# Performance work log

Measured on AMD Instinct MI355X. Metric: run time of the kernel, lower is better.

The kernel has to match this reference:

```python
import jax, jax.numpy as jnp
import numpy as np

N_NODES = 100000
NEG_SLOPE = 0.2


def gat_conv(x, src, dst, W, a_src, a_dst, bias, concat):
    """PyG-style GATConv (eval mode, self-loops assumed already added).
    x: [N, F_in], src/dst: [E] (message flows src -> dst).
    W: [F_in, H*C], a_src/a_dst: [H, C], bias: [H*C] or [C].
    """
    H, C = a_src.shape
    N = x.shape[0]
    h = (x @ W).reshape(N, H, C)                      # [N, H, C]
    alpha_src = jnp.einsum('nhc,hc->nh', h, a_src)    # [N, H]
    alpha_dst = jnp.einsum('nhc,hc->nh', h, a_dst)    # [N, H]
    e = jax.nn.leaky_relu(alpha_src[src] + alpha_dst[dst], NEG_SLOPE)  # [E, H]
    # segment softmax over incoming edges of each dst node
    e_max = jax.ops.segment_max(e, dst, num_segments=N)
    e_exp = jnp.exp(e - e_max[dst])
    denom = jax.ops.segment_sum(e_exp, dst, num_segments=N)
    alpha = e_exp / (denom[dst] + 1e-16)              # [E, H]
    msg = h[src] * alpha[:, :, None]                  # [E, H, C]
    out = jax.ops.segment_sum(msg, dst, num_segments=N)  # [N, H, C]
    out = out.reshape(N, H * C) if concat else out.mean(axis=1)
    return out + bias


def add_self_loops(edge_index, n):
    loop = jnp.arange(n, dtype=edge_index.dtype)
    src = jnp.concatenate([edge_index[0], loop])
    dst = jnp.concatenate([edge_index[1], loop])
    return src, dst


def setup_inputs() -> dict:
    key = jax.random.key(0)
    ks = jax.random.split(key, 10)
    F_in, H1, C1, n_cls = 128, 8, 8, 40
    E = 1600000
    x = jax.random.normal(ks[0], (N_NODES, F_in), dtype=jnp.float32)
    edge_index = jax.random.randint(ks[1], (2, E), 0, N_NODES, dtype=jnp.int64)
    g = lambda k, shp, fan: jax.random.normal(k, shp, dtype=jnp.float32) * (1.0 / np.sqrt(fan))
    return {
        'x': x,
        'edge_index': edge_index,
        'W1': g(ks[2], (F_in, H1 * C1), F_in),
        'a_src1': g(ks[3], (H1, C1), C1),
        'a_dst1': g(ks[4], (H1, C1), C1),
        'b1': jnp.zeros((H1 * C1,), dtype=jnp.float32),
        'W2': g(ks[5], (H1 * C1, n_cls), H1 * C1),
        'a_src2': g(ks[6], (1, n_cls), n_cls),
        'a_dst2': g(ks[7], (1, n_cls), n_cls),
        'b2': jnp.zeros((n_cls,), dtype=jnp.float32),
    }


def reference(x, edge_index, W1, a_src1, a_dst1, b1, W2, a_src2, a_dst2, b2):
    src, dst = add_self_loops(edge_index, N_NODES)
    # dropout(p=0.6) layers are identity in eval mode
    h = gat_conv(x, src, dst, W1, a_src1, a_dst1, b1, concat=True)
    h = jax.nn.relu(h)
    out = gat_conv(h, src, dst, W2, a_src2, a_dst2, b2, concat=True)
    return out
```

## Files before the change

kernel.cpp:

```cpp
#include <hip/hip_runtime.h>
#include <math.h>

constexpr int NN     = 100000;
constexpr int E_BASE = 1600000;
constexpr int E_TOT  = E_BASE + NN;
constexpr int F_IN   = 128;
constexpr int F1     = 64;
constexpr int H1n    = 8;
constexpr int F2     = 40;

constexpr int BSHIFT    = 9;
constexpr int NB        = (NN + 511) >> BSHIFT;
constexpr int BCAP      = 12288;
constexpr int P1_BLOCKS = 256;
constexpr int EPB       = (E_TOT + P1_BLOCKS - 1) / P1_BLOCKS;
constexpr int L1_BLOCKS = (NN + 63) / 64;

__device__ __forceinline__ float lrelu(float v) { return fmaxf(v, 0.2f * v); }

__device__ __forceinline__ unsigned bpack(float a, float b) {
    unsigned ua = __float_as_uint(a) + 0x8000u;
    unsigned ub = __float_as_uint(b) + 0x8000u;
    return (ua >> 16) | (ub & 0xFFFF0000u);
}
__device__ __forceinline__ float blo(unsigned u) { return __uint_as_float(u << 16); }
__device__ __forceinline__ float bhi(unsigned u) { return __uint_as_float(u & 0xFFFF0000u); }

__global__ __launch_bounds__(256) void fused_l1p(const float* __restrict__ x,
                                                 const float* __restrict__ W1,
                                                 const float* __restrict__ a_src,
                                                 const float* __restrict__ a_dst,
                                                 unsigned* __restrict__ h1b,
                                                 float* __restrict__ as1,
                                                 float* __restrict__ ad1,
                                                 const int* __restrict__ src,
                                                 const int* __restrict__ dst,
                                                 int* __restrict__ bucket_cnt,
                                                 unsigned* __restrict__ store) {
    __shared__ __align__(16) unsigned char smraw[17408];
    int t = threadIdx.x;
    if (blockIdx.x < L1_BLOCKS) {
        float (*xs)[36] = (float(*)[36])smraw;
        float* wsld     = (float*)(smraw + 9216);
        int nb = blockIdx.x * 64;
        int ct = t & 15, nt = t >> 4;
        int rs = t >> 3, qs = t & 7;
        float acc[4][4] = {};
        for (int K0 = 0; K0 < F_IN; K0 += 32) {
            int r0 = min(nb + rs, NN - 1);
            int r1 = min(nb + rs + 32, NN - 1);
            float4 v0 = *(const float4*)&x[(size_t)r0 * F_IN + K0 + qs * 4];
            float4 v1 = *(const float4*)&x[(size_t)r1 * F_IN + K0 + qs * 4];
            *(float4*)&xs[rs][qs * 4] = v0;
            *(float4*)&xs[rs + 32][qs * 4] = v1;
            const float4* wsrc = (const float4*)&W1[(size_t)K0 * F1];
            *(float4*)&wsld[t * 4] = wsrc[t];
            *(float4*)&wsld[1024 + t * 4] = wsrc[256 + t];
            __syncthreads();
#pragma unroll 8
            for (int kk = 0; kk < 32; ++kk) {
                float4 w = *(const float4*)&wsld[kk * 64 + ct * 4];
                float x0 = xs[nt * 4 + 0][kk];
                float x1 = xs[nt * 4 + 1][kk];
                float x2 = xs[nt * 4 + 2][kk];
                float x3 = xs[nt * 4 + 3][kk];
                acc[0][0] = fmaf(x0, w.x, acc[0][0]); acc[0][1] = fmaf(x0, w.y, acc[0][1]);
                acc[0][2] = fmaf(x0, w.z, acc[0][2]); acc[0][3] = fmaf(x0, w.w, acc[0][3]);
                acc[1][0] = fmaf(x1, w.x, acc[1][0]); acc[1][1] = fmaf(x1, w.y, acc[1][1]);
                acc[1][2] = fmaf(x1, w.z, acc[1][2]); acc[1][3] = fmaf(x1, w.w, acc[1][3]);
                acc[2][0] = fmaf(x2, w.x, acc[2][0]); acc[2][1] = fmaf(x2, w.y, acc[2][1]);
                acc[2][2] = fmaf(x2, w.z, acc[2][2]); acc[2][3] = fmaf(x2, w.w, acc[2][3]);
                acc[3][0] = fmaf(x3, w.x, acc[3][0]); acc[3][1] = fmaf(x3, w.y, acc[3][1]);
                acc[3][2] = fmaf(x3, w.z, acc[3][2]); acc[3][3] = fmaf(x3, w.w, acc[3][3]);
            }
            __syncthreads();
        }
        float4 as4 = ((const float4*)a_src)[ct];
        float4 ds4 = ((const float4*)a_dst)[ct];
#pragma unroll
        for (int i = 0; i < 4; ++i) {
            int n = nb + nt * 4 + i;
            unsigned u0 = bpack(acc[i][0], acc[i][1]);
            unsigned u1 = bpack(acc[i][2], acc[i][3]);
            float ps = acc[i][0]*as4.x + acc[i][1]*as4.y + acc[i][2]*as4.z + acc[i][3]*as4.w;
            float pd = acc[i][0]*ds4.x + acc[i][1]*ds4.y + acc[i][2]*ds4.z + acc[i][3]*ds4.w;
            ps += __shfl_xor(ps, 1, 64);
            pd += __shfl_xor(pd, 1, 64);
            if (n < NN) {
                *(uint2*)&h1b[(size_t)n * 32 + ct * 2] = make_uint2(u0, u1);
                if (!(ct & 1)) {
                    as1[n * H1n + (ct >> 1)] = ps;
                    ad1[n * H1n + (ct >> 1)] = pd;
                }
            }
        }
    } else {
        int* bins  = (int*)smraw;
        int* basep = (int*)(smraw + NB * 4);
        for (int i = t; i < NB; i += 256) bins[i] = 0;
        __syncthreads();
        int pb = blockIdx.x - L1_BLOCKS;
        int e0 = pb * EPB;
        int e1 = min(e0 + EPB, E_TOT);
        for (int e = e0 + t; e < e1; e += 256) {
            int d = (e < E_BASE) ? dst[e] : (e - E_BASE);
            atomicAdd(&bins[d >> BSHIFT], 1);
        }
        __syncthreads();
        for (int i = t; i < NB; i += 256) {
            basep[i] = atomicAdd(&bucket_cnt[i], bins[i]);
            bins[i] = 0;
        }
        __syncthreads();
        for (int e = e0 + t; e < e1; e += 256) {
            int s, d;
            if (e < E_BASE) { s = src[e]; d = dst[e]; }
            else            { s = e - E_BASE; d = s; }
            int b = d >> BSHIFT;
            int p = atomicAdd(&bins[b], 1);
            store[(size_t)b * BCAP + basep[b] + p] = ((unsigned)s << 9) | (unsigned)(d & 511);
        }
    }
}

__global__ __launch_bounds__(256) void bucket_csr(const int* __restrict__ bucket_cnt,
                                                  const unsigned* __restrict__ store,
                                                  int* __restrict__ row_start,
                                                  int* __restrict__ csr_src) {
    __shared__ int cnt_l[512];
    __shared__ int incl[512];
    __shared__ int cur_l[512];
    __shared__ int sh_gbase;
    int b = blockIdx.x;
    int t = threadIdx.x;
    int cnt = bucket_cnt[b];
    int nlo = b << BSHIFT;
    int nodes = min(512, NN - nlo);
    cnt_l[t] = 0; cnt_l[t + 256] = 0;
    if (t < 64) {
        int partial = 0;
        for (int i = t; i < NB; i += 64)
            if (i < b) partial += bucket_cnt[i];
#pragma unroll
        for (int m = 1; m < 64; m <<= 1) partial += __shfl_xor(partial, m, 64);
        if (t == 0) {
            sh_gbase = partial;
            if (b == NB - 1) row_start[NN] = partial + cnt;
        }
    }
    __syncthreads();
    int gbase = sh_gbase;
    const unsigned* sp = store + (size_t)b * BCAP;
    for (int i = t; i < cnt; i += 256)
        atomicAdd(&cnt_l[sp[i] & 511], 1);
    __syncthreads();
    if (t < 64) {
        int run = 0;
        for (int c = 0; c < 512; c += 64) {
            int v = cnt_l[c + t];
#pragma unroll
            for (int off = 1; off < 64; off <<= 1) {
                int u = __shfl_up(v, off, 64);
                if (t >= off) v += u;
            }
            incl[c + t] = run + v;
            run = __shfl(run + v, 63, 64);
        }
    }
    __syncthreads();
    for (int j = t; j < 512; j += 256) {
        int start = gbase + incl[j] - cnt_l[j];
        cur_l[j] = start;
        if (j < nodes) row_start[nlo + j] = start;
    }
    __syncthreads();
    for (int i = t; i < cnt; i += 256) {
        unsigned ed = sp[i];
        int p = atomicAdd(&cur_l[ed & 511], 1);
        csr_src[p] = (int)(ed >> 9);
    }
}

__global__ void node_agg1(const int* __restrict__ row_start, const int* __restrict__ csr_src,
                          const float* __restrict__ as1, const float* __restrict__ ad1,
                          const unsigned* __restrict__ h1b, const float* __restrict__ b1,
                          float* __restrict__ out1r) {
    int n = blockIdx.x;
    int lane = threadIdx.x;
    int e8 = lane & 7, hp = lane >> 3;
    int il = lane & 31, q = lane >> 5;
    int hc = il >> 2;
    float adv = ad1[n * H1n + hp];
    int lo = row_start[n], hi = row_start[n + 1];
    float ssum = 0.f, acc0 = 0.f, acc1 = 0.f;
    for (int base = lo; base < hi; base += 8) {
        int idx = base + e8;
        bool valid = idx < hi;
        int s = csr_src[valid ? idx : (hi - 1)];
        float v = lrelu(as1[s * H1n + hp] + adv);
        float p = valid ? __expf(v) : 0.f;
        ssum += p;
#pragma unroll
        for (int j = 0; j < 4; ++j) {
            int e = 2 * j + q;
            int   sb = __shfl(s, e, 64);
            float pb = __shfl(p, (hc << 3) | e, 64);
            unsigned u = h1b[(size_t)sb * 32 + il];
            acc0 = fmaf(pb, blo(u), acc0);
            acc1 = fmaf(pb, bhi(u), acc1);
        }
    }
    ssum += __shfl_xor(ssum, 1, 64);
    ssum += __shfl_xor(ssum, 2, 64);
    ssum += __shfl_xor(ssum, 4, 64);
    float sh = __shfl(ssum, hc << 3, 64);
    float p0 = acc0 + __shfl(acc0, il | 32, 64);
    float p1 = acc1 + __shfl(acc1, il | 32, 64);
    if (lane < 32) {
        float r = 1.f / (sh + 1e-16f);
        float2 bv = ((const float2*)b1)[il];
        float2 o;
        o.x = fmaxf(fmaf(p0, r, bv.x), 0.f);
        o.y = fmaxf(fmaf(p1, r, bv.y), 0.f);
        ((float2*)(out1r + (size_t)n * F1))[il] = o;
    }
}

__global__ __launch_bounds__(256) void linear2(const float* __restrict__ out1r,
                                               const float* __restrict__ W2,
                                               const float* __restrict__ a_src2,
                                               const float* __restrict__ a_dst2,
                                               unsigned* __restrict__ h2a,
                                               unsigned* __restrict__ h2c,
                                               float* __restrict__ as2,
                                               float* __restrict__ ad2) {
    __shared__ float xs[128][65];
    __shared__ float ws[64 * 40];
    int t = threadIdx.x;
    int nb = blockIdx.x * 128;
    int colq = t & 15, rr = t >> 4;
#pragma unroll
    for (int i = 0; i < 8; ++i) {
        int r = rr + 16 * i;
        int g = min(nb + r, NN - 1);
        float4 v = *(const float4*)&out1r[(size_t)g * F1 + colq * 4];
        xs[r][colq * 4 + 0] = v.x; xs[r][colq * 4 + 1] = v.y;
        xs[r][colq * 4 + 2] = v.z; xs[r][colq * 4 + 3] = v.w;
    }
#pragma unroll
    for (int i = 0; i < 10; ++i) ws[t + 256 * i] = W2[t + 256 * i];
    __syncthreads();
    int ct = t & 7, nt = t >> 3;
    float acc[4][5] = {};
#pragma unroll 4
    for (int k = 0; k < F1; ++k) {
        float w0 = ws[k * 40 + ct * 5 + 0];
        float w1 = ws[k * 40 + ct * 5 + 1];
        float w2 = ws[k * 40 + ct * 5 + 2];
        float w3 = ws[k * 40 + ct * 5 + 3];
        float w4 = ws[k * 40 + ct * 5 + 4];
#pragma unroll
        for (int i = 0; i < 4; ++i) {
            float xv = xs[nt * 4 + i][k];
            acc[i][0] = fmaf(xv, w0, acc[i][0]);
            acc[i][1] = fmaf(xv, w1, acc[i][1]);
            acc[i][2] = fmaf(xv, w2, acc[i][2]);
            acc[i][3] = fmaf(xv, w3, acc[i][3]);
            acc[i][4] = fmaf(xv, w4, acc[i][4]);
        }
    }
    float aw[5], dw[5];
#pragma unroll
    for (int j = 0; j < 5; ++j) { aw[j] = a_src2[ct * 5 + j]; dw[j] = a_dst2[ct * 5 + j]; }
#pragma unroll
    for (int i = 0; i < 4; ++i) {
        int n = nb + nt * 4 + i;
        float vs = acc[i][0]*aw[0] + acc[i][1]*aw[1] + acc[i][2]*aw[2]
                 + acc[i][3]*aw[3] + acc[i][4]*aw[4];
        float vd = acc[i][0]*dw[0] + acc[i][1]*dw[1] + acc[i][2]*dw[2]
                 + acc[i][3]*dw[3] + acc[i][4]*dw[4];
        vs += __shfl_xor(vs, 1, 64); vs += __shfl_xor(vs, 2, 64); vs += __shfl_xor(vs, 4, 64);
        vd += __shfl_xor(vd, 1, 64); vd += __shfl_xor(vd, 2, 64); vd += __shfl_xor(vd, 4, 64);
        if (n < NN && ct == 0) { as2[n] = vs; ad2[n] = vd; }
    }
    __syncthreads();
#pragma unroll
    for (int i = 0; i < 4; ++i) {
        int r = nt * 4 + i;
#pragma unroll
        for (int j = 0; j < 5; ++j) xs[r][ct * 5 + j] = acc[i][j];
    }
    __syncthreads();
    {
        int r = t >> 1, half = t & 1;
        int n = nb + r;
        if (n < NN) {
#pragma unroll
            for (int k = 0; k < 10; ++k) {
                int w = half * 10 + k;
                unsigned val = bpack(xs[r][2 * w], xs[r][2 * w + 1]);
                if (w < 16) h2a[(size_t)n * 16 + w] = val;
                else        h2c[(size_t)n * 4 + (w - 16)] = val;
            }
        }
    }
}

__global__ void node_agg2(const int* __restrict__ row_start, const int* __restrict__ csr_src,
                          const float* __restrict__ as2, const float* __restrict__ ad2,
                          const unsigned* __restrict__ h2a, const unsigned* __restrict__ h2c,
                          const float* __restrict__ b2, float* __restrict__ out) {
    int n = blockIdx.x;
    int lane = threadIdx.x;
    int e8 = lane & 7;
    int il = lane & 31, q = lane >> 5;
    bool act = il < 20;
    const unsigned* gbase;
    unsigned gstride;
    if (il < 16)      { gbase = h2a + il;        gstride = 16u; }
    else if (il < 20) { gbase = h2c + (il - 16); gstride = 4u;  }
    else              { gbase = h2c;             gstride = 0u;  }
    float adv = ad2[n];
    int lo = row_start[n], hi = row_start[n + 1];
    float ssum = 0.f, acc0 = 0.f, acc1 = 0.f;
    for (int base = lo; base < hi; base += 8) {
        int idx = base + e8;
        bool valid = idx < hi;
        int s = csr_src[valid ? idx : (hi - 1)];
        float v = lrelu(as2[s] + adv);
        float p = valid ? __expf(v) : 0.f;
        ssum += p;
#pragma unroll
        for (int j = 0; j < 4; ++j) {
            int e = 2 * j + q;
            int   sb = __shfl(s, e, 64);
            float pb = __shfl(p, e, 64);
            unsigned u = gbase[(size_t)((unsigned)sb * gstride)];
            acc0 = fmaf(pb, blo(u), acc0);
            acc1 = fmaf(pb, bhi(u), acc1);
        }
    }
    ssum += __shfl_xor(ssum, 1, 64);
    ssum += __shfl_xor(ssum, 2, 64);
    ssum += __shfl_xor(ssum, 4, 64);
    float p0 = acc0 + __shfl(acc0, il | 32, 64);
    float p1 = acc1 + __shfl(acc1, il | 32, 64);
    if (lane < 32 && act) {
        float r = 1.f / (ssum + 1e-16f);
        float2 bv = ((const float2*)b2)[il];
        float2 o;
        o.x = fmaf(p0, r, bv.x);
        o.y = fmaf(p1, r, bv.y);
        ((float2*)(out + (size_t)n * F2))[il] = o;
    }
}

extern "C" void kernel_launch(void* const* d_in, const int* in_sizes, int n_in,
                              void* d_out, int out_size, void* d_ws, size_t ws_size,
                              hipStream_t stream) {
    const float* x      = (const float*)d_in[0];
    const int*   ei     = (const int*)d_in[1];
    const float* W1     = (const float*)d_in[2];
    const float* a_src1 = (const float*)d_in[3];
    const float* a_dst1 = (const float*)d_in[4];
    const float* b1     = (const float*)d_in[5];
    const float* W2     = (const float*)d_in[6];
    const float* a_src2 = (const float*)d_in[7];
    const float* a_dst2 = (const float*)d_in[8];
    const float* b2     = (const float*)d_in[9];
    float* out = (float*)d_out;
    const int* srcp = ei;
    const int* dstp = ei + E_BASE;

    unsigned* h1b        = (unsigned*)d_ws;
    unsigned* storeu     = h1b + (size_t)NN * 32;
    float*    as1        = (float*)(storeu + (size_t)NB * BCAP);
    float*    ad1        = as1 + (size_t)NN * H1n;
    float*    out1r      = ad1 + (size_t)NN * H1n;
    unsigned* h2a        = (unsigned*)(out1r + (size_t)NN * F1);
    unsigned* h2c        = h2a + (size_t)NN * 16;
    float*    as2        = (float*)(h2c + (size_t)NN * 4);
    float*    ad2        = as2 + NN;
    int*      row_start  = (int*)(ad2 + NN);
    int*      csr_src    = row_start + (NN + 1);
    int*      bucket_cnt = csr_src + E_TOT;

    hipMemsetAsync(bucket_cnt, 0, NB * sizeof(int), stream);

    fused_l1p<<<L1_BLOCKS + P1_BLOCKS, 256, 0, stream>>>(
        x, W1, a_src1, a_dst1, h1b, as1, ad1, srcp, dstp, bucket_cnt, storeu);
    bucket_csr<<<NB, 256, 0, stream>>>(bucket_cnt, storeu, row_start, csr_src);

    node_agg1<<<NN, 64, 0, stream>>>(row_start, csr_src, as1, ad1, h1b, b1, out1r);

    linear2<<<(NN + 127) / 128, 256, 0, stream>>>(out1r, W2, a_src2, a_dst2, h2a, h2c, as2, ad2);
    node_agg2<<<NN, 64, 0, stream>>>(row_start, csr_src, as2, ad2, h2a, h2c, b2, out);
}
```

Baseline: 191.9 us.

## Pack four nodes per block and prefetch next edge chunk in aggregation kernels

Result: slower. 201.6 us (+5.1%).

```diff
diff --git a/kernel.cpp b/kernel.cpp
--- a/kernel.cpp
+++ b/kernel.cpp
@@ -181,34 +181,44 @@
     }
 }
 
-__global__ void node_agg1(const int* __restrict__ row_start, const int* __restrict__ csr_src,
-                          const float* __restrict__ as1, const float* __restrict__ ad1,
-                          const unsigned* __restrict__ h1b, const float* __restrict__ b1,
-                          float* __restrict__ out1r) {
-    int n = blockIdx.x;
-    int lane = threadIdx.x;
+__global__ __launch_bounds__(256) void node_agg1(const int* __restrict__ row_start,
+                                                 const int* __restrict__ csr_src,
+                                                 const float* __restrict__ as1,
+                                                 const float* __restrict__ ad1,
+                                                 const unsigned* __restrict__ h1b,
+                                                 const float* __restrict__ b1,
+                                                 float* __restrict__ out1r) {
+    int n = blockIdx.x * 4 + (threadIdx.x >> 6);
+    if (n >= NN) return;
+    int lane = threadIdx.x & 63;
     int e8 = lane & 7, hp = lane >> 3;
     int il = lane & 31, q = lane >> 5;
     int hc = il >> 2;
-    float adv = ad1[n * H1n + hp];
+    float adv = ad1[(unsigned)n * 8u + (unsigned)hp];
     int lo = row_start[n], hi = row_start[n + 1];
     float ssum = 0.f, acc0 = 0.f, acc1 = 0.f;
+    int   s_cur = csr_src[(unsigned)min(lo + e8, hi - 1)];
+    float g_cur = as1[(unsigned)s_cur * 8u + (unsigned)hp];
     for (int base = lo; base < hi; base += 8) {
-        int idx = base + e8;
-        bool valid = idx < hi;
-        int s = csr_src[valid ? idx : (hi - 1)];
-        float v = lrelu(as1[s * H1n + hp] + adv);
-        float p = valid ? __expf(v) : 0.f;
+        int nb2 = base + 8;
+        int s_nxt = s_cur; float g_nxt = 0.f;
+        if (nb2 < hi) {
+            s_nxt = csr_src[(unsigned)min(nb2 + e8, hi - 1)];
+            g_nxt = as1[(unsigned)s_nxt * 8u + (unsigned)hp];
+        }
+        float v = lrelu(g_cur + adv);
+        float p = (base + e8 < hi) ? __expf(v) : 0.f;
         ssum += p;
 #pragma unroll
         for (int j = 0; j < 4; ++j) {
             int e = 2 * j + q;
-            int   sb = __shfl(s, e, 64);
+            int   sb = __shfl(s_cur, e, 64);
             float pb = __shfl(p, (hc << 3) | e, 64);
-            unsigned u = h1b[(size_t)sb * 32 + il];
+            unsigned u = h1b[(unsigned)sb * 32u + (unsigned)il];
             acc0 = fmaf(pb, blo(u), acc0);
             acc1 = fmaf(pb, bhi(u), acc1);
         }
+        s_cur = s_nxt; g_cur = g_nxt;
     }
     ssum += __shfl_xor(ssum, 1, 64);
     ssum += __shfl_xor(ssum, 2, 64);
@@ -306,39 +316,47 @@
     }
 }
 
-__global__ void node_agg2(const int* __restrict__ row_start, const int* __restrict__ csr_src,
-                          const float* __restrict__ as2, const float* __restrict__ ad2,
-                          const unsigned* __restrict__ h2a, const unsigned* __restrict__ h2c,
-                          const float* __restrict__ b2, float* __restrict__ out) {
-    int n = blockIdx.x;
-    int lane = threadIdx.x;
+__global__ __launch_bounds__(256) void node_agg2(const int* __restrict__ row_start,
+                                                 const int* __restrict__ csr_src,
+                                                 const float* __restrict__ as2,
+                                                 const float* __restrict__ ad2,
+                                                 const unsigned* __restrict__ h2,
+                                                 const float* __restrict__ b2,
+                                                 float* __restrict__ out) {
+    int n = blockIdx.x * 4 + (threadIdx.x >> 6);
+    if (n >= NN) return;
+    int lane = threadIdx.x & 63;
     int e8 = lane & 7;
     int il = lane & 31, q = lane >> 5;
     bool act = il < 20;
-    const unsigned* gbase;
-    unsigned gstride;
-    if (il < 16)      { gbase = h2a + il;        gstride = 16u; }
-    else if (il < 20) { gbase = h2c + (il - 16); gstride = 4u;  }
-    else              { gbase = h2c;             gstride = 0u;  }
+    unsigned gstride = (il < 16) ? 16u : ((il < 20) ? 4u : 0u);
+    unsigned gofs    = (il < 16) ? (unsigned)il
+                     : ((il < 20) ? (unsigned)(NN * 16 + (il - 16)) : 0u);
     float adv = ad2[n];
     int lo = row_start[n], hi = row_start[n + 1];
     float ssum = 0.f, acc0 = 0.f, acc1 = 0.f;
+    int   s_cur = csr_src[(unsigned)min(lo + e8, hi - 1)];
+    float g_cur = as2[(unsigned)s_cur];
     for (int base = lo; base < hi; base += 8) {
-        int idx = base + e8;
-        bool valid = idx < hi;
-        int s = csr_src[valid ? idx : (hi - 1)];
-        float v = lrelu(as2[s] + adv);
-        float p = valid ? __expf(v) : 0.f;
+        int nb2 = base + 8;
+        int s_nxt = s_cur; float g_nxt = 0.f;
+        if (nb2 < hi) {
+            s_nxt = csr_src[(unsigned)min(nb2 + e8, hi - 1)];
+            g_nxt = as2[(unsigned)s_nxt];
+        }
+        float v = lrelu(g_cur + adv);
+        float p = (base + e8 < hi) ? __expf(v) : 0.f;
         ssum += p;
 #pragma unroll
         for (int j = 0; j < 4; ++j) {
             int e = 2 * j + q;
-            int   sb = __shfl(s, e, 64);
+            int   sb = __shfl(s_cur, e, 64);
             float pb = __shfl(p, e, 64);
-            unsigned u = gbase[(size_t)((unsigned)sb * gstride)];
+            unsigned u = h2[(unsigned)sb * gstride + gofs];
             acc0 = fmaf(pb, blo(u), acc0);
             acc1 = fmaf(pb, bhi(u), acc1);
         }
+        s_cur = s_nxt; g_cur = g_nxt;
     }
     ssum += __shfl_xor(ssum, 1, 64);
     ssum += __shfl_xor(ssum, 2, 64);
@@ -391,8 +409,8 @@
         x, W1, a_src1, a_dst1, h1b, as1, ad1, srcp, dstp, bucket_cnt, storeu);
     bucket_csr<<<NB, 256, 0, stream>>>(bucket_cnt, storeu, row_start, csr_src);
 
-    node_agg1<<<NN, 64, 0, stream>>>(row_start, csr_src, as1, ad1, h1b, b1, out1r);
+    node_agg1<<<(NN + 3) / 4, 256, 0, stream>>>(row_start, csr_src, as1, ad1, h1b, b1, out1r);
 
     linear2<<<(NN + 127) / 128, 256, 0, stream>>>(out1r, W2, a_src2, a_dst2, h2a, h2c, as2, ad2);
-    node_agg2<<<NN, 64, 0, stream>>>(row_start, csr_src, as2, ad2, h2a, h2c, b2, out);
-}
+    node_agg2<<<(NN + 3) / 4, 256, 0, stream>>>(row_start, csr_src, as2, ad2, h2a, b2, out);
+}
```
